# Kernel tuning notes

Measured on AMD Instinct MI355X. Metric: run time of the kernel, lower is better.

## Reference

```python
import jax, jax.numpy as jnp
import numpy as np

VOCAB = 8192
DIM = 64
COMMITMENT = 0.25
N = 65536


def setup_inputs() -> dict:
    key = jax.random.key(0)
    kx, ke = jax.random.split(key)
    x = jax.random.normal(kx, (N, DIM), dtype=jnp.float32)
    # matches nn.Embedding weight init uniform_(-0.5, 0.5)
    emb_weight = jax.random.uniform(ke, (VOCAB, DIM), dtype=jnp.float32, minval=-0.5, maxval=0.5)
    return {"x": x, "emb_weight": emb_weight}


def reference(x, emb_weight):
    # cdist(x, E, p=2): squared form gives identical argmin (sqrt is monotone)
    x2 = jnp.sum(x * x, axis=-1, keepdims=True)            # [N, 1]
    e2 = jnp.sum(emb_weight * emb_weight, axis=-1)         # [V]
    d2 = x2 + e2[None, :] - 2.0 * (x @ emb_weight.T)       # [N, V]
    idx = jnp.argmin(d2, axis=-1)                          # [N] int

    quantised = emb_weight[idx]                            # [N, D] gather

    codebook_loss = jnp.mean((quantised - jax.lax.stop_gradient(x)) ** 2)
    e_latent_loss = jnp.mean((jax.lax.stop_gradient(quantised) - x) ** 2)
    loss = codebook_loss + COMMITMENT * e_latent_loss

    # straight-through estimator
    quantised_ste = x + jax.lax.stop_gradient(quantised - x)
    return quantised_ste, loss, idx
```

## Files before the change

kernel.cpp:

```cpp
#include <hip/hip_runtime.h>

#define N 65536
#define D 64
#define V 8192
#define LOSS_OFF (N * D)
#define IDX_OFF (N * D + 1)
#define MARGIN 0.02f
#define NPART 4

typedef _Float16 half8 __attribute__((ext_vector_type(8)));
typedef float f32x4 __attribute__((ext_vector_type(4)));

typedef __attribute__((address_space(1))) const void gas_t;
typedef __attribute__((address_space(3))) void las_t;

#define DOT16(s, A0, A1, A2, A3, B0, B1, B2, B3)                         \
    s = fmaf(A0.x, B0.x, s); s = fmaf(A0.y, B0.y, s);                    \
    s = fmaf(A0.z, B0.z, s); s = fmaf(A0.w, B0.w, s);                    \
    s = fmaf(A1.x, B1.x, s); s = fmaf(A1.y, B1.y, s);                    \
    s = fmaf(A1.z, B1.z, s); s = fmaf(A1.w, B1.w, s);                    \
    s = fmaf(A2.x, B2.x, s); s = fmaf(A2.y, B2.y, s);                    \
    s = fmaf(A2.z, B2.z, s); s = fmaf(A2.w, B2.w, s);                    \
    s = fmaf(A3.x, B3.x, s); s = fmaf(A3.y, B3.y, s);                    \
    s = fmaf(A3.z, B3.z, s); s = fmaf(A3.w, B3.w, s);

__device__ __forceinline__ unsigned enc32(float f) {
    unsigned u = __float_as_uint(f);
    return (u & 0x80000000u) ? ~u : (u | 0x80000000u);
}

__global__ __launch_bounds__(256) void k_split(const float* __restrict__ E,
                                               _Float16* __restrict__ Ef16,
                                               float* __restrict__ e2,
                                               float* __restrict__ dout,
                                               int* __restrict__ fcount) {
    const int t = blockIdx.x * 256 + threadIdx.x;
    if (t == 0) {
        dout[LOSS_OFF] = 0.0f;
        *fcount = 0;
    }
    const int row = t >> 3;
    const int seg = t & 7;
    const float4* p = (const float4*)(E + (size_t)row * D + seg * 8);
    float4 a = p[0], b = p[1];
    float s = a.x * a.x + a.y * a.y + a.z * a.z + a.w * a.w +
              b.x * b.x + b.y * b.y + b.z * b.z + b.w * b.w;
    s += __shfl_xor(s, 1, 8);
    s += __shfl_xor(s, 2, 8);
    s += __shfl_xor(s, 4, 8);
    if (seg == 0) e2[row] = s;
    half8 h;
    h[0] = (_Float16)(-2.0f * a.x); h[1] = (_Float16)(-2.0f * a.y);
    h[2] = (_Float16)(-2.0f * a.z); h[3] = (_Float16)(-2.0f * a.w);
    h[4] = (_Float16)(-2.0f * b.x); h[5] = (_Float16)(-2.0f * b.y);
    h[6] = (_Float16)(-2.0f * b.z); h[7] = (_Float16)(-2.0f * b.w);
    *(half8*)(Ef16 + (size_t)row * D + seg * 8) = h;
}

#define MERGE(M1, M2, GID, L, PID)          \
    {                                       \
        bool bt = (L) < (M1);               \
        float m2c = bt ? (M1) : (L);        \
        (M2) = fminf((M2), m2c);            \
        (GID) = bt ? (PID) : (GID);         \
        (M1) = fminf((M1), (L));            \
    }

__global__ __launch_bounds__(512) void k_argmin(const float* __restrict__ X,
                                                const _Float16* __restrict__ Ef16,
                                                const float* __restrict__ e2,
                                                float4* __restrict__ part4) {
    __shared__ __align__(16) _Float16 els[2][8192];

    const int tid = threadIdx.x;
    const int lane = tid & 63;
    const int wave = tid >> 6;
    const int P = blockIdx.x & 3;
    const int rb = blockIdx.x >> 2;
    const int c4 = lane & 15;
    const int kg = lane >> 4;
    const int wrow = rb * 256 + wave * 32;
    const int sw = c4 & 7;
    const int k0off = (kg ^ sw) * 8;
    const int k1off = ((4 + kg) ^ sw) * 8;
    const int ch0 = P * 16;

    half8 x00, x01, x10, x11;
    {
        const float* xr0 = X + (size_t)(wrow + c4) * D;
        const float* xr1 = X + (size_t)(wrow + 16 + c4) * D;
#pragma unroll
        for (int f = 0; f < 2; ++f) {
            float4 lo = *(const float4*)(xr0 + f * 32 + kg * 8);
            float4 hi = *(const float4*)(xr0 + f * 32 + kg * 8 + 4);
            half8 h;
            h[0] = (_Float16)lo.x; h[1] = (_Float16)lo.y;
            h[2] = (_Float16)lo.z; h[3] = (_Float16)lo.w;
            h[4] = (_Float16)hi.x; h[5] = (_Float16)hi.y;
            h[6] = (_Float16)hi.z; h[7] = (_Float16)hi.w;
            if (f == 0) x00 = h; else x01 = h;
        }
#pragma unroll
        for (int f = 0; f < 2; ++f) {
            float4 lo = *(const float4*)(xr1 + f * 32 + kg * 8);
            float4 hi = *(const float4*)(xr1 + f * 32 + kg * 8 + 4);
            half8 h;
            h[0] = (_Float16)lo.x; h[1] = (_Float16)lo.y;
            h[2] = (_Float16)lo.z; h[3] = (_Float16)lo.w;
            h[4] = (_Float16)hi.x; h[5] = (_Float16)hi.y;
            h[6] = (_Float16)hi.z; h[7] = (_Float16)hi.w;
            if (f == 0) x10 = h; else x11 = h;
        }
    }

    const int q0 = tid, q1 = tid + 512;
    const _Float16* gs0 = Ef16 + (size_t)(ch0 * 128 + (q0 >> 3)) * 64 + ((q0 & 7) ^ ((q0 >> 3) & 7)) * 8;
    const _Float16* gs1 = Ef16 + (size_t)(ch0 * 128 + (q1 >> 3)) * 64 + ((q1 & 7) ^ ((q1 >> 3) & 7)) * 8;
    const int ld0 = q0 * 8, ld1 = q1 * 8;

#define STAGE(BUF)                                                            \
    {                                                                         \
        __builtin_amdgcn_global_load_lds((gas_t*)gs0, (las_t*)&els[BUF][ld0], 16, 0, 0); \
        __builtin_amdgcn_global_load_lds((gas_t*)gs1, (las_t*)&els[BUF][ld1], 16, 0, 0); \
        gs0 += 8192; gs1 += 8192;                                             \
    }

    float m1a = 3.4e38f, m2a = 3.4e38f, m1b = 3.4e38f, m2b = 3.4e38f;
    unsigned gida = 0, gidb = 0;
    const unsigned kgu = (unsigned)kg;

#define TSTEP(T, E2Q)                                                         \
    {                                                                         \
        const half8 a0 = *(const half8*)&els[buf][(T * 16 + c4) * 64 + k0off];\
        const half8 a1 = *(const half8*)&els[buf][(T * 16 + c4) * 64 + k1off];\
        f32x4 acc0 = __builtin_amdgcn_mfma_f32_16x16x32_f16(a0, x00, E2Q, 0, 0, 0); \
        acc0 = __builtin_amdgcn_mfma_f32_16x16x32_f16(a1, x01, acc0, 0, 0, 0);\
        f32x4 acc1 = __builtin_amdgcn_mfma_f32_16x16x32_f16(a0, x10, E2Q, 0, 0, 0); \
        acc1 = __builtin_amdgcn_mfma_f32_16x16x32_f16(a1, x11, acc1, 0, 0, 0);\
        La = fminf(fminf(fminf(fminf(La, acc0[0]), acc0[1]), acc0[2]), acc0[3]); \
        Lb = fminf(fminf(fminf(fminf(Lb, acc1[0]), acc1[1]), acc1[2]), acc1[3]); \
    }

    STAGE(0)
    const f32x4* e2p = (const f32x4*)(e2 + (size_t)ch0 * 128) + kg;

    for (int ci = 0; ci < 16; ++ci) {
        __syncthreads();
        const f32x4 e2q0 = e2p[0],  e2q1 = e2p[4],  e2q2 = e2p[8],  e2q3 = e2p[12];
        const f32x4 e2q4 = e2p[16], e2q5 = e2p[20], e2q6 = e2p[24], e2q7 = e2p[28];
        e2p += 32;
        if (ci < 15) STAGE((ci + 1) & 1)
        const int buf = ci & 1;

        float La = 3.4e38f, Lb = 3.4e38f;
        TSTEP(0, e2q0) TSTEP(1, e2q1) TSTEP(2, e2q2) TSTEP(3, e2q3)
        TSTEP(4, e2q4) TSTEP(5, e2q5) TSTEP(6, e2q6) TSTEP(7, e2q7)

        unsigned pid = (unsigned)((ch0 + ci) * 4) + kgu;
        MERGE(m1a, m2a, gida, La, pid)
        MERGE(m1b, m2b, gidb, Lb, pid)
    }

#pragma unroll
    for (int off = 16; off < 64; off <<= 1) {
        float o1, o2;
        unsigned og;
        o1 = __shfl_xor(m1a, off, 64); o2 = __shfl_xor(m2a, off, 64);
        og = (unsigned)__shfl_xor((int)gida, off, 64);
        m2a = fminf(fminf(fmaxf(m1a, o1), m2a), o2);
        if (o1 < m1a) gida = og;
        m1a = fminf(m1a, o1);
        o1 = __shfl_xor(m1b, off, 64); o2 = __shfl_xor(m2b, off, 64);
        og = (unsigned)__shfl_xor((int)gidb, off, 64);
        m2b = fminf(fminf(fmaxf(m1b, o1), m2b), o2);
        if (o1 < m1b) gidb = og;
        m1b = fminf(m1b, o1);
    }

    if (lane < 16) {
        float4 r;
        r.x = m1a; r.y = m2a; r.z = __uint_as_float(gida); r.w = 0.0f;
        part4[(size_t)P * N + wrow + lane] = r;
        r.x = m1b; r.y = m2b; r.z = __uint_as_float(gidb);
        part4[(size_t)P * N + wrow + 16 + lane] = r;
    }
}

__global__ __launch_bounds__(256) void k_group(const float* __restrict__ X,
                                               const float* __restrict__ E,
                                               const float* __restrict__ e2,
                                               const float4* __restrict__ part4,
                                               int* __restrict__ fcount,
                                               int* __restrict__ flist,
                                               unsigned long long* __restrict__ packed,
                                               float* __restrict__ lpart,
                                               float* __restrict__ dout) {
    const int lane = threadIdx.x & 63;
    const int wave = threadIdx.x >> 6;
    const int row = blockIdx.x * 4 + wave;

    float m1, m2;
    unsigned g;
    {
        const float4 r0 = part4[row];
        m1 = r0.x; m2 = r0.y; g = __float_as_uint(r0.z);
#pragma unroll
        for (int k = 1; k < NPART; ++k) {
            const float4 r = part4[(size_t)k * N + row];
            const unsigned rg = __float_as_uint(r.z);
            if (r.x < m1) {
                m2 = fminf(m2, m1);
                m1 = r.x;
                g = rg;
            } else {
                m2 = fminf(m2, r.x);
            }
            m2 = fminf(m2, r.y);
        }
    }

    float lossp = 0.0f;
    if (m2 - m1 < MARGIN) {
        if (lane == 0) {
            int p = atomicAdd(fcount, 1);
            flist[p] = row;
            packed[p] = ~0ull;
        }
    } else {
        const int ch = (int)(g >> 2);
        const int kgr = (int)(g & 3);
        const int e4 = lane >> 2;
        const int dg = lane & 3;
        const float4* xp = (const float4*)(X + (size_t)row * D) + dg * 4;
        float4 xa0 = xp[0], xa1 = xp[1], xa2 = xp[2], xa3 = xp[3];

        float best = 3.4e38f;
        int bidx = 0x7fffffff;
#pragma unroll
        for (int it = 0; it < 2; ++it) {
            const int s = it * 16 + e4;
            const int v = ch * 128 + ((s >> 2) << 4) + kgr * 4 + (s & 3);
            const float4* ep = (const float4*)(E + (size_t)v * D) + dg * 4;
            float4 b0 = ep[0], b1 = ep[1], b2 = ep[2], b3 = ep[3];
            float s0 = 0.0f;
            DOT16(s0, xa0, xa1, xa2, xa3, b0, b1, b2, b3)
            s0 += __shfl_xor(s0, 1, 64);
            s0 += __shfl_xor(s0, 2, 64);
            float d = fmaf(-2.0f, s0, e2[v]);
            if (d < best) { best = d; bidx = v; }
        }
#pragma unroll
        for (int off = 4; off < 64; off <<= 1) {
            float ob = __shfl_xor(best, off, 64);
            int oi = __shfl_xor(bidx, off, 64);
            if (ob < best || (ob == best && oi < bidx)) { best = ob; bidx = oi; }
        }
        if (lane == 0) dout[IDX_OFF + row] = (float)bidx;
        if (lane < 16) {
            float4 x4 = *(const float4*)(X + (size_t)row * D + lane * 4);
            float4 q4 = *(const float4*)(E + (size_t)bidx * D + lane * 4);
            float4 o;
            o.x = x4.x + (q4.x - x4.x);
            o.y = x4.y + (q4.y - x4.y);
            o.z = x4.z + (q4.z - x4.z);
            o.w = x4.w + (q4.w - x4.w);
            *(float4*)(dout + (size_t)row * D + lane * 4) = o;
            float dx = q4.x - x4.x, dy = q4.y - x4.y, dz = q4.z - x4.z,
                  dw = q4.w - x4.w;
            lossp = dx * dx + dy * dy + dz * dz + dw * dw;
        }
    }

#pragma unroll
    for (int off = 32; off; off >>= 1) lossp += __shfl_down(lossp, off, 64);
    __shared__ float ps[4];
    if (lane == 0) ps[wave] = lossp;
    __syncthreads();
    if (threadIdx.x == 0) lpart[blockIdx.x] = ps[0] + ps[1] + ps[2] + ps[3];
}

__global__ __launch_bounds__(256) void k_full(const float* __restrict__ X,
                                              const float* __restrict__ E,
                                              const float* __restrict__ e2,
                                              const int* __restrict__ fcount,
                                              const int* __restrict__ flist,
                                              unsigned long long* __restrict__ packed) {
    const int nf = *fcount;
    if (nf == 0) return;
    const int nq = (nf + 3) >> 2;
    const int total = nq * 8;
    const int lane = threadIdx.x & 63;
    const int nwaves = gridDim.x * 4;
    int item = blockIdx.x * 4 + (threadIdx.x >> 6);
    const int e4 = lane >> 2;
    const int dg = lane & 3;

    for (; item < total; item += nwaves) {
        const int qi = item >> 3;
        const int c = item & 7;
        const int f0 = qi * 4;
        const int f1 = min(f0 + 1, nf - 1);
        const int f2 = min(f0 + 2, nf - 1);
        const int f3 = min(f0 + 3, nf - 1);
        const int r0 = flist[f0], r1 = flist[f1], r2 = flist[f2], r3 = flist[f3];

        const float4* xp0 = (const float4*)(X + (size_t)r0 * D) + dg * 4;
        const float4* xp1 = (const float4*)(X + (size_t)r1 * D) + dg * 4;
        const float4* xp2 = (const float4*)(X + (size_t)r2 * D) + dg * 4;
        const float4* xp3 = (const float4*)(X + (size_t)r3 * D) + dg * 4;
        float4 xa0 = xp0[0], xa1 = xp0[1], xa2 = xp0[2], xa3 = xp0[3];
        float4 xb0 = xp1[0], xb1 = xp1[1], xb2 = xp1[2], xb3 = xp1[3];
        float4 xc0 = xp2[0], xc1 = xp2[1], xc2 = xp2[2], xc3 = xp2[3];
        float4 xd0 = xp3[0], xd1 = xp3[1], xd2 = xp3[2], xd3 = xp3[3];

        unsigned long long k0 = ~0ull, k1 = ~0ull, k2 = ~0ull, k3 = ~0ull;

#pragma unroll 2
        for (int it = 0; it < 64; ++it) {
            const int v = c * 1024 + it * 16 + e4;
            const float4* ep = (const float4*)(E + (size_t)v * D) + dg * 4;
            float4 b0 = ep[0], b1 = ep[1], b2 = ep[2], b3 = ep[3];
            float s0 = 0.0f, s1 = 0.0f, s2 = 0.0f, s3 = 0.0f;
            DOT16(s0, xa0, xa1, xa2, xa3, b0, b1, b2, b3)
            DOT16(s1, xb0, xb1, xb2, xb3, b0, b1, b2, b3)
            DOT16(s2, xc0, xc1, xc2, xc3, b0, b1, b2, b3)
            DOT16(s3, xd0, xd1, xd2, xd3, b0, b1, b2, b3)
            s0 += __shfl_xor(s0, 1, 64); s0 += __shfl_xor(s0, 2, 64);
            s1 += __shfl_xor(s1, 1, 64); s1 += __shfl_xor(s1, 2, 64);
            s2 += __shfl_xor(s2, 1, 64); s2 += __shfl_xor(s2, 2, 64);
            s3 += __shfl_xor(s3, 1, 64); s3 += __shfl_xor(s3, 2, 64);
            const float ev = e2[v];
            const unsigned long long vb = (unsigned long long)(unsigned)v;
            unsigned long long t;
            t = ((unsigned long long)enc32(fmaf(-2.0f, s0, ev)) << 32) | vb;
            k0 = t < k0 ? t : k0;
            t = ((unsigned long long)enc32(fmaf(-2.0f, s1, ev)) << 32) | vb;
            k1 = t < k1 ? t : k1;
            t = ((unsigned long long)enc32(fmaf(-2.0f, s2, ev)) << 32) | vb;
            k2 = t < k2 ? t : k2;
            t = ((unsigned long long)enc32(fmaf(-2.0f, s3, ev)) << 32) | vb;
            k3 = t < k3 ? t : k3;
        }

#pragma unroll
        for (int off = 4; off < 64; off <<= 1) {
            unsigned lo, hi;
            unsigned long long o;
            lo = __shfl_xor((unsigned)k0, off, 64); hi = __shfl_xor((unsigned)(k0 >> 32), off, 64);
            o = ((unsigned long long)hi << 32) | lo; k0 = o < k0 ? o : k0;
            lo = __shfl_xor((unsigned)k1, off, 64); hi = __shfl_xor((unsigned)(k1 >> 32), off, 64);
            o = ((unsigned long long)hi << 32) | lo; k1 = o < k1 ? o : k1;
            lo = __shfl_xor((unsigned)k2, off, 64); hi = __shfl_xor((unsigned)(k2 >> 32), off, 64);
            o = ((unsigned long long)hi << 32) | lo; k2 = o < k2 ? o : k2;
            lo = __shfl_xor((unsigned)k3, off, 64); hi = __shfl_xor((unsigned)(k3 >> 32), off, 64);
            o = ((unsigned long long)hi << 32) | lo; k3 = o < k3 ? o : k3;
        }

        if (lane == 0) {
            atomicMin(&packed[f0], k0);
            atomicMin(&packed[f1], k1);
            atomicMin(&packed[f2], k2);
            atomicMin(&packed[f3], k3);
        }
    }
}

__global__ __launch_bounds__(256) void k_out2(const float* __restrict__ X,
                                              const float* __restrict__ E,
                                              const int* __restrict__ fcount,
                                              const int* __restrict__ flist,
                                              const unsigned long long* __restrict__ packed,
                                              const float* __restrict__ lpart,
                                              float* __restrict__ dout) {
    const int lane = threadIdx.x & 63;
    const int wave = threadIdx.x >> 6;
    float lossp = 0.0f;
    if (wave == 0) lossp += lpart[blockIdx.x * 64 + lane];

    const int nf = *fcount;
    const int nwaves = gridDim.x * 4;
    for (int i = blockIdx.x * 4 + wave; i < nf; i += nwaves) {
        const int row = flist[i];
        const int idx = (int)(unsigned)(packed[i] & 0xffffffffull);
        if (lane == 0) dout[IDX_OFF + row] = (float)idx;
        if (lane < 16) {
            float4 x4 = *(const float4*)(X + (size_t)row * D + lane * 4);
            float4 q4 = *(const float4*)(E + (size_t)idx * D + lane * 4);
            float4 o;
            o.x = x4.x + (q4.x - x4.x);
            o.y = x4.y + (q4.y - x4.y);
            o.z = x4.z + (q4.z - x4.z);
            o.w = x4.w + (q4.w - x4.w);
            *(float4*)(dout + (size_t)row * D + lane * 4) = o;
            float dx = q4.x - x4.x, dy = q4.y - x4.y, dz = q4.z - x4.z,
                  dw = q4.w - x4.w;
            lossp += dx * dx + dy * dy + dz * dz + dw * dw;
        }
    }

#pragma unroll
    for (int off = 32; off; off >>= 1) lossp += __shfl_down(lossp, off, 64);
    __shared__ float ps[4];
    if (lane == 0) ps[wave] = lossp;
    __syncthreads();
    if (threadIdx.x == 0) {
        float tot = ps[0] + ps[1] + ps[2] + ps[3];
        atomicAdd(dout + LOSS_OFF, tot * (1.25f / ((float)N * (float)D)));
    }
}

extern "C" void kernel_launch(void* const* d_in, const int* in_sizes, int n_in,
                              void* d_out, int out_size, void* d_ws,
                              size_t ws_size, hipStream_t stream) {
    const float* X = (const float*)d_in[0];
    const float* E = (const float*)d_in[1];
    float* out = (float*)d_out;

    char* ws = (char*)d_ws;
    _Float16* Ef16 = (_Float16*)ws;
    float* e2 = (float*)(ws + 1048576);
    int* fcount = (int*)(ws + 1081344);
    int* flist = (int*)(ws + 1081600);
    unsigned long long* packed = (unsigned long long*)(ws + 1343744);
    float* lpart = (float*)(ws + 1868032);
    float4* part4 = (float4*)(ws + 1933568);

    k_split<<<256, 256, 0, stream>>>(E, Ef16, e2, out, fcount);
    k_argmin<<<(N / 256) * NPART, 512, 0, stream>>>(X, Ef16, e2, part4);
    k_group<<<N / 4, 256, 0, stream>>>(X, E, e2, part4, fcount, flist, packed, lpart, out);
    k_full<<<1024, 256, 0, stream>>>(X, E, e2, fcount, flist, packed);
    k_out2<<<256, 256, 0, stream>>>(X, E, fcount, flist, packed, lpart, out);
}
```

Baseline: 199.8 us.

## Track argmin per 4-code group and refine with 16 lanes per row

The argmin kernel now merges top-2 minima after every 16-column tile instead of once per 128-code chunk, so the winning group id narrows to 4 codes rather than 32. The group refinement kernel then needs only one fp32 dot per code, which lets each wave handle four rows with 16 lanes each. The grid shrinks fourfold and the loss-partial count shrinks with it, so k_out2 is launched with fewer blocks. In exchange, the MFMA inner loop takes more compare/select work per tile.

After: 174.8 us. -12.5%, faster.

```diff
diff --git a/kernel.cpp b/kernel.cpp
--- a/kernel.cpp
+++ b/kernel.cpp
@@ -127,7 +127,6 @@
 
     float m1a = 3.4e38f, m2a = 3.4e38f, m1b = 3.4e38f, m2b = 3.4e38f;
     unsigned gida = 0, gidb = 0;
-    const unsigned kgu = (unsigned)kg;
 
 #define TSTEP(T, E2Q)                                                         \
     {                                                                         \
@@ -137,12 +136,16 @@
         acc0 = __builtin_amdgcn_mfma_f32_16x16x32_f16(a1, x01, acc0, 0, 0, 0);\
         f32x4 acc1 = __builtin_amdgcn_mfma_f32_16x16x32_f16(a0, x10, E2Q, 0, 0, 0); \
         acc1 = __builtin_amdgcn_mfma_f32_16x16x32_f16(a1, x11, acc1, 0, 0, 0);\
-        La = fminf(fminf(fminf(fminf(La, acc0[0]), acc0[1]), acc0[2]), acc0[3]); \
-        Lb = fminf(fminf(fminf(fminf(Lb, acc1[0]), acc1[1]), acc1[2]), acc1[3]); \
+        float Lq0 = fminf(fminf(acc0[0], acc0[1]), fminf(acc0[2], acc0[3]));  \
+        float Lq1 = fminf(fminf(acc1[0], acc1[1]), fminf(acc1[2], acc1[3]));  \
+        const unsigned pid = pidq + T * 4;                                    \
+        MERGE(m1a, m2a, gida, Lq0, pid)                                       \
+        MERGE(m1b, m2b, gidb, Lq1, pid)                                       \
     }
 
     STAGE(0)
     const f32x4* e2p = (const f32x4*)(e2 + (size_t)ch0 * 128) + kg;
+    unsigned pidq = (unsigned)(ch0 * 32 + kg);
 
     for (int ci = 0; ci < 16; ++ci) {
         __syncthreads();
@@ -152,13 +155,9 @@
         if (ci < 15) STAGE((ci + 1) & 1)
         const int buf = ci & 1;
 
-        float La = 3.4e38f, Lb = 3.4e38f;
         TSTEP(0, e2q0) TSTEP(1, e2q1) TSTEP(2, e2q2) TSTEP(3, e2q3)
         TSTEP(4, e2q4) TSTEP(5, e2q5) TSTEP(6, e2q6) TSTEP(7, e2q7)
-
-        unsigned pid = (unsigned)((ch0 + ci) * 4) + kgu;
-        MERGE(m1a, m2a, gida, La, pid)
-        MERGE(m1b, m2b, gidb, Lb, pid)
+        pidq += 32;
     }
 
 #pragma unroll
@@ -197,7 +196,9 @@
                                                float* __restrict__ dout) {
     const int lane = threadIdx.x & 63;
     const int wave = threadIdx.x >> 6;
-    const int row = blockIdx.x * 4 + wave;
+    const int lig = lane & 15;
+    const int grp = lane >> 4;
+    const int row = blockIdx.x * 16 + wave * 4 + grp;
 
     float m1, m2;
     unsigned g;
@@ -221,54 +222,43 @@
 
     float lossp = 0.0f;
     if (m2 - m1 < MARGIN) {
-        if (lane == 0) {
+        if (lig == 0) {
             int p = atomicAdd(fcount, 1);
             flist[p] = row;
             packed[p] = ~0ull;
         }
     } else {
-        const int ch = (int)(g >> 2);
-        const int kgr = (int)(g & 3);
-        const int e4 = lane >> 2;
-        const int dg = lane & 3;
+        const int e = lig >> 2;
+        const int dg = lig & 3;
+        const int v = (int)(g << 2) + e;
         const float4* xp = (const float4*)(X + (size_t)row * D) + dg * 4;
         float4 xa0 = xp[0], xa1 = xp[1], xa2 = xp[2], xa3 = xp[3];
-
-        float best = 3.4e38f;
-        int bidx = 0x7fffffff;
-#pragma unroll
-        for (int it = 0; it < 2; ++it) {
-            const int s = it * 16 + e4;
-            const int v = ch * 128 + ((s >> 2) << 4) + kgr * 4 + (s & 3);
-            const float4* ep = (const float4*)(E + (size_t)v * D) + dg * 4;
-            float4 b0 = ep[0], b1 = ep[1], b2 = ep[2], b3 = ep[3];
-            float s0 = 0.0f;
-            DOT16(s0, xa0, xa1, xa2, xa3, b0, b1, b2, b3)
-            s0 += __shfl_xor(s0, 1, 64);
-            s0 += __shfl_xor(s0, 2, 64);
-            float d = fmaf(-2.0f, s0, e2[v]);
-            if (d < best) { best = d; bidx = v; }
-        }
-#pragma unroll
-        for (int off = 4; off < 64; off <<= 1) {
-            float ob = __shfl_xor(best, off, 64);
+        const float4* ep = (const float4*)(E + (size_t)v * D) + dg * 4;
+        float4 b0 = ep[0], b1 = ep[1], b2 = ep[2], b3 = ep[3];
+        float s = 0.0f;
+        DOT16(s, xa0, xa1, xa2, xa3, b0, b1, b2, b3)
+        s += __shfl_xor(s, 1, 64);
+        s += __shfl_xor(s, 2, 64);
+        float d = fmaf(-2.0f, s, e2[v]);
+        int bidx = v;
+#pragma unroll
+        for (int off = 4; off < 16; off <<= 1) {
+            float ob = __shfl_xor(d, off, 64);
             int oi = __shfl_xor(bidx, off, 64);
-            if (ob < best || (ob == best && oi < bidx)) { best = ob; bidx = oi; }
-        }
-        if (lane == 0) dout[IDX_OFF + row] = (float)bidx;
-        if (lane < 16) {
-            float4 x4 = *(const float4*)(X + (size_t)row * D + lane * 4);
-            float4 q4 = *(const float4*)(E + (size_t)bidx * D + lane * 4);
-            float4 o;
-            o.x = x4.x + (q4.x - x4.x);
-            o.y = x4.y + (q4.y - x4.y);
-            o.z = x4.z + (q4.z - x4.z);
-            o.w = x4.w + (q4.w - x4.w);
-            *(float4*)(dout + (size_t)row * D + lane * 4) = o;
-            float dx = q4.x - x4.x, dy = q4.y - x4.y, dz = q4.z - x4.z,
-                  dw = q4.w - x4.w;
-            lossp = dx * dx + dy * dy + dz * dz + dw * dw;
-        }
+            if (ob < d || (ob == d && oi < bidx)) { d = ob; bidx = oi; }
+        }
+        if (lig == 0) dout[IDX_OFF + row] = (float)bidx;
+        float4 x4 = *(const float4*)(X + (size_t)row * D + lig * 4);
+        float4 q4 = *(const float4*)(E + (size_t)bidx * D + lig * 4);
+        float4 o;
+        o.x = x4.x + (q4.x - x4.x);
+        o.y = x4.y + (q4.y - x4.y);
+        o.z = x4.z + (q4.z - x4.z);
+        o.w = x4.w + (q4.w - x4.w);
+        *(float4*)(dout + (size_t)row * D + lig * 4) = o;
+        float dx = q4.x - x4.x, dy = q4.y - x4.y, dz = q4.z - x4.z,
+              dw = q4.w - x4.w;
+        lossp = dx * dx + dy * dy + dz * dz + dw * dw;
     }
 
 #pragma unroll
@@ -427,7 +417,7 @@
 
     k_split<<<256, 256, 0, stream>>>(E, Ef16, e2, out, fcount);
     k_argmin<<<(N / 256) * NPART, 512, 0, stream>>>(X, Ef16, e2, part4);
-    k_group<<<N / 4, 256, 0, stream>>>(X, E, e2, part4, fcount, flist, packed, lpart, out);
+    k_group<<<N / 16, 256, 0, stream>>>(X, E, e2, part4, fcount, flist, packed, lpart, out);
     k_full<<<1024, 256, 0, stream>>>(X, E, e2, fcount, flist, packed);
-    k_out2<<<256, 256, 0, stream>>>(X, E, fcount, flist, packed, lpart, out);
-}
+    k_out2<<<64, 256, 0, stream>>>(X, E, fcount, flist, packed, lpart, out);
+}
```
